# Optimization experiments

Measured on AMD Instinct MI355X. Metric: run time of the kernel, lower is better.

## Reference

```python
import jax, jax.numpy as jnp
import numpy as np

N_NODES = 100000
N_EDGES = 1000000
D_FEAT = 64
N_GRAPHS = 64


def setup_inputs() -> dict:
    key = jax.random.key(0)
    ks = jax.random.split(key, 5)
    x = jax.random.normal(ks[0], (N_NODES, D_FEAT), dtype=jnp.float32)
    edge_index = jax.random.randint(ks[1], (2, N_EDGES), 0, N_NODES, dtype=jnp.int32)
    batch = jnp.sort(jax.random.randint(ks[2], (N_NODES,), 0, N_GRAPHS, dtype=jnp.int32))
    s = 1.0 / np.sqrt(D_FEAT)
    W1 = jax.random.uniform(ks[3], (D_FEAT, D_FEAT), jnp.float32, -s, s)
    W2 = jax.random.uniform(ks[4], (D_FEAT, D_FEAT), jnp.float32, -s, s)
    b1 = jnp.zeros((D_FEAT,), jnp.float32)
    b2 = jnp.zeros((D_FEAT,), jnp.float32)
    return {"x": x, "edge_index": edge_index, "batch": batch,
            "W1": W1, "b1": b1, "W2": W2, "b2": b2}


def gcn_conv(x, edge_index, W, b, num_nodes):
    # PyG GCNConv: h = D^{-1/2} (A + I) D^{-1/2} (x W) + b
    loops = jnp.arange(num_nodes, dtype=edge_index.dtype)
    row = jnp.concatenate([edge_index[0], loops])  # source nodes
    col = jnp.concatenate([edge_index[1], loops])  # target nodes
    h = x @ W  # [N, D]
    deg = jax.ops.segment_sum(jnp.ones_like(col, dtype=h.dtype), col,
                              num_segments=num_nodes)  # >= 1 due to self loops
    dinv = jax.lax.rsqrt(deg)
    norm = dinv[row] * dinv[col]  # [E+N]
    out = jax.ops.segment_sum(h[row] * norm[:, None], col, num_segments=num_nodes)
    return out + b


def reference(x, edge_index, batch, W1, b1, W2, b2):
    n = x.shape[0]
    h = gcn_conv(x, edge_index, W1, b1, n)
    h = gcn_conv(h, edge_index, W2, b2, n)
    # global_mean_pool over graph ids
    sums = jax.ops.segment_sum(h, batch, num_segments=N_GRAPHS)  # [G, D]
    cnts = jax.ops.segment_sum(jnp.ones((n, 1), h.dtype), batch,
                               num_segments=N_GRAPHS)
    return sums / jnp.maximum(cnts, 1.0)
```

## Files before the change

### kernel.cpp

```cpp
#include <hip/hip_runtime.h>
#include <hip/hip_fp16.h>

#define DFEAT 64
#define NG 64
#define TILE 128
#define NBLK 256
#define NBMAX 1024

__global__ __launch_bounds__(256) void k_cnt(const int* __restrict__ col,
                                             int* __restrict__ cnt_m,
                                             float* __restrict__ zeroreg,
                                             const float* __restrict__ x,
                                             __half2* __restrict__ xh,
                                             int e, int nb, int chunk, int n32) {
  __shared__ int hist[NBMAX];
  int tid = threadIdx.x;
  int blk = blockIdx.x;
  if (blk == 0) {
    for (int i = tid; i < 4224; i += 256) zeroreg[i] = 0.f;
  }
  for (int b = tid; b < nb; b += 256) hist[b] = 0;
  __syncthreads();
  int lo = blk * chunk, hi = min(lo + chunk, e);
  for (int i = lo + tid; i < hi; i += 256)
    atomicAdd(&hist[col[i] >> 7], 1);
  __syncthreads();
  for (int b = tid; b < nb; b += 256)
    cnt_m[(size_t)blk * nb + b] = hist[b];
  for (int i = blk * 256 + tid; i < n32; i += NBLK * 256) {
    float2 v = ((const float2*)x)[i];
    xh[i] = __float22half2_rn(v);
  }
}

__global__ __launch_bounds__(256) void k_colscan(int* __restrict__ cnt_m,
                                                 int* __restrict__ gcount, int nb) {
  __shared__ int sh[256];
  int tid = threadIdx.x;
  int b = blockIdx.x;
  int v = cnt_m[(size_t)tid * nb + b];
  sh[tid] = v;
  __syncthreads();
  for (int off = 1; off < 256; off <<= 1) {
    int t = (tid >= off) ? sh[tid - off] : 0;
    __syncthreads();
    sh[tid] += t;
    __syncthreads();
  }
  cnt_m[(size_t)tid * nb + b] = sh[tid] - v;
  if (tid == 255) gcount[b] = sh[255];
}

__global__ __launch_bounds__(1024) void k_bscan(const int* __restrict__ gcount,
                                                int* __restrict__ base, int nb,
                                                const float* __restrict__ W1,
                                                const float* __restrict__ W2,
                                                const float* __restrict__ b1,
                                                float* __restrict__ WW,
                                                float* __restrict__ bw) {
  __shared__ int sh[1024];
  __shared__ float w1[4096], w2[4096];
  int tid = threadIdx.x;
  if (blockIdx.x == 0) {
    int v = (tid < nb) ? gcount[tid] : 0;
    sh[tid] = v;
    __syncthreads();
    for (int off = 1; off < 1024; off <<= 1) {
      int t = (tid >= off) ? sh[tid - off] : 0;
      __syncthreads();
      sh[tid] += t;
      __syncthreads();
    }
    if (tid < nb) base[tid] = sh[tid] - v;
    if (tid == 0) base[nb] = sh[1023];
  } else {
    for (int i = tid; i < 4096; i += 1024) { w1[i] = W1[i]; w2[i] = W2[i]; }
    __syncthreads();
    for (int p = tid; p < 4096; p += 1024) {
      int k = p >> 6, d = p & 63;
      float a = 0.f;
      for (int m = 0; m < 64; ++m) a += w1[k * 64 + m] * w2[m * 64 + d];
      WW[p] = a;
    }
    if (tid < 64) {
      float a = 0.f;
      for (int k = 0; k < 64; ++k) a += b1[k] * w2[k * 64 + tid];
      bw[tid] = a;
    }
  }
}

__global__ __launch_bounds__(256) void k_bin2(const int* __restrict__ row,
                                              const int* __restrict__ col,
                                              const int* __restrict__ base,
                                              const int* __restrict__ cnt_m,
                                              int* __restrict__ pairs,
                                              int e, int nb, int chunk) {
  __shared__ int gl[NBMAX];
  __shared__ int lcur[NBMAX];
  int tid = threadIdx.x;
  int blk = blockIdx.x;
  for (int b = tid; b < nb; b += 256) {
    gl[b] = base[b] + cnt_m[(size_t)blk * nb + b];
    lcur[b] = 0;
  }
  __syncthreads();
  int lo = blk * chunk, hi = min(lo + chunk, e);
  for (int i = lo + tid; i < hi; i += 256) {
    int s = row[i], t = col[i];
    int b = t >> 7;
    int pos = gl[b] + atomicAdd(&lcur[b], 1);
    pairs[pos] = s | ((t & (TILE - 1)) << 20);
  }
}

__global__ __launch_bounds__(256) void k_csr(const int* __restrict__ pairs,
                                             const int* __restrict__ base,
                                             int* __restrict__ starts,
                                             int* __restrict__ srcs,
                                             float* __restrict__ dinv,
                                             int n, int e) {
  __shared__ int cnt[TILE];
  __shared__ int cur[TILE];
  __shared__ int sc[TILE];
  int tid = threadIdx.x;
  int b = blockIdx.x;
  int tile0 = b * TILE;
  if (tid < TILE) cnt[tid] = 0;
  __syncthreads();
  int e0 = base[b], e1 = base[b + 1];
  for (int i = e0 + tid; i < e1; i += 256)
    atomicAdd(&cnt[(unsigned)pairs[i] >> 20], 1);
  __syncthreads();
  int c = (tid < TILE) ? cnt[tid] : 0;
  if (tid < TILE) sc[tid] = c;
  __syncthreads();
  for (int off = 1; off < TILE; off <<= 1) {
    int t = (tid < TILE && tid >= off) ? sc[tid - off] : 0;
    __syncthreads();
    if (tid < TILE) sc[tid] += t;
    __syncthreads();
  }
  if (tid < TILE) {
    int excl = sc[tid] - c;
    cur[tid] = excl;
    int node = tile0 + tid;
    if (node < n) {
      starts[node] = e0 + excl;
      dinv[node] = rsqrtf(1.0f + (float)c);
    }
  }
  if (b == 0 && tid == 0) starts[n] = e;
  __syncthreads();
  for (int i = e0 + tid; i < e1; i += 256) {
    int p = pairs[i];
    int pos = atomicAdd(&cur[(unsigned)p >> 20], 1);
    srcs[e0 + pos] = p & 0xFFFFF;
  }
}

__global__ __launch_bounds__(256) void k_gather1(const int* __restrict__ starts,
                                                 const int* __restrict__ srcs,
                                                 const float* __restrict__ dinv,
                                                 const __half2* __restrict__ xh,
                                                 __half2* __restrict__ z1h,
                                                 float* __restrict__ u, int n) {
  int node = blockIdx.x * 8 + (threadIdx.x >> 5);
  if (node >= n) return;
  int lh = threadIdx.x & 31;
  int s = starts[node];
  int deg = starts[node + 1] - s;
  float dc = dinv[node];
  float2 hs = __half22float2(xh[(size_t)node * 32 + lh]);
  float ax = 0.f, ay = 0.f, wsum = 0.f;
  int j = 0;
  for (; j + 7 < deg; j += 8) {
    int r0 = srcs[s + j + 0], r1 = srcs[s + j + 1];
    int r2 = srcs[s + j + 2], r3 = srcs[s + j + 3];
    int r4 = srcs[s + j + 4], r5 = srcs[s + j + 5];
    int r6 = srcs[s + j + 6], r7 = srcs[s + j + 7];
    float w0 = dinv[r0], w1 = dinv[r1], w2 = dinv[r2], w3 = dinv[r3];
    float w4 = dinv[r4], w5 = dinv[r5], w6 = dinv[r6], w7 = dinv[r7];
    float2 v0 = __half22float2(xh[(size_t)r0 * 32 + lh]);
    float2 v1 = __half22float2(xh[(size_t)r1 * 32 + lh]);
    float2 v2 = __half22float2(xh[(size_t)r2 * 32 + lh]);
    float2 v3 = __half22float2(xh[(size_t)r3 * 32 + lh]);
    float2 v4 = __half22float2(xh[(size_t)r4 * 32 + lh]);
    float2 v5 = __half22float2(xh[(size_t)r5 * 32 + lh]);
    float2 v6 = __half22float2(xh[(size_t)r6 * 32 + lh]);
    float2 v7 = __half22float2(xh[(size_t)r7 * 32 + lh]);
    ax += w0 * v0.x + w1 * v1.x + w2 * v2.x + w3 * v3.x
        + w4 * v4.x + w5 * v5.x + w6 * v6.x + w7 * v7.x;
    ay += w0 * v0.y + w1 * v1.y + w2 * v2.y + w3 * v3.y
        + w4 * v4.y + w5 * v5.y + w6 * v6.y + w7 * v7.y;
    wsum += w0 + w1 + w2 + w3 + w4 + w5 + w6 + w7;
  }
  for (; j < deg; ++j) {
    int r = srcs[s + j];
    float w = dinv[r];
    float2 v = __half22float2(xh[(size_t)r * 32 + lh]);
    ax += w * v.x;
    ay += w * v.y;
    wsum += w;
  }
  float2 res;
  res.x = dc * dc * hs.x + dc * ax;
  res.y = dc * dc * hs.y + dc * ay;
  z1h[(size_t)node * 32 + lh] = __float22half2_rn(res);
  if (lh == 0) u[node] = dc * (dc + wsum);
}

__global__ __launch_bounds__(256) void k_gather2(const int* __restrict__ starts,
                                                 const int* __restrict__ srcs,
                                                 const float* __restrict__ dinv,
                                                 const __half2* __restrict__ z1h,
                                                 float* __restrict__ z2, int n) {
  int node = blockIdx.x * 8 + (threadIdx.x >> 5);
  if (node >= n) return;
  int lh = threadIdx.x & 31;
  int s = starts[node];
  int deg = starts[node + 1] - s;
  float dc = dinv[node];
  float2 hs = __half22float2(z1h[(size_t)node * 32 + lh]);
  float ax = 0.f, ay = 0.f;
  int j = 0;
  for (; j + 7 < deg; j += 8) {
    int r0 = srcs[s + j + 0], r1 = srcs[s + j + 1];
    int r2 = srcs[s + j + 2], r3 = srcs[s + j + 3];
    int r4 = srcs[s + j + 4], r5 = srcs[s + j + 5];
    int r6 = srcs[s + j + 6], r7 = srcs[s + j + 7];
    float w0 = dinv[r0], w1 = dinv[r1], w2 = dinv[r2], w3 = dinv[r3];
    float w4 = dinv[r4], w5 = dinv[r5], w6 = dinv[r6], w7 = dinv[r7];
    float2 v0 = __half22float2(z1h[(size_t)r0 * 32 + lh]);
    float2 v1 = __half22float2(z1h[(size_t)r1 * 32 + lh]);
    float2 v2 = __half22float2(z1h[(size_t)r2 * 32 + lh]);
    float2 v3 = __half22float2(z1h[(size_t)r3 * 32 + lh]);
    float2 v4 = __half22float2(z1h[(size_t)r4 * 32 + lh]);
    float2 v5 = __half22float2(z1h[(size_t)r5 * 32 + lh]);
    float2 v6 = __half22float2(z1h[(size_t)r6 * 32 + lh]);
    float2 v7 = __half22float2(z1h[(size_t)r7 * 32 + lh]);
    ax += w0 * v0.x + w1 * v1.x + w2 * v2.x + w3 * v3.x
        + w4 * v4.x + w5 * v5.x + w6 * v6.x + w7 * v7.x;
    ay += w0 * v0.y + w1 * v1.y + w2 * v2.y + w3 * v3.y
        + w4 * v4.y + w5 * v5.y + w6 * v6.y + w7 * v7.y;
  }
  for (; j < deg; ++j) {
    int r = srcs[s + j];
    float w = dinv[r];
    float2 v = __half22float2(z1h[(size_t)r * 32 + lh]);
    ax += w * v.x;
    ay += w * v.y;
  }
  float2 res;
  res.x = dc * dc * hs.x + dc * ax;
  res.y = dc * dc * hs.y + dc * ay;
  *(float2*)(&z2[(size_t)node * 64 + lh * 2]) = res;
}

__global__ void k_pool2(const float* __restrict__ z2, const float* __restrict__ u,
                        const int* __restrict__ batch, float* __restrict__ S,
                        float* __restrict__ T, float* __restrict__ cntf, int n) {
  int d = threadIdx.x;
  int start = blockIdx.x * 64;
  if (start >= n) return;
  int end = min(start + 64, n);
  int curg = batch[start];
  float acc = 0.f, cnt = 0.f, ua = 0.f;
  for (int i = start; i < end; ++i) {
    int g = batch[i];
    if (g != curg) {
      unsafeAtomicAdd(&S[curg * 64 + d], acc);
      if (d == 0) {
        unsafeAtomicAdd(&cntf[curg], cnt);
        unsafeAtomicAdd(&T[curg], ua);
      }
      acc = 0.f; cnt = 0.f; ua = 0.f;
      curg = g;
    }
    acc += z2[(size_t)i * 64 + d];
    if (d == 0) { cnt += 1.f; ua += u[i]; }
  }
  unsafeAtomicAdd(&S[curg * 64 + d], acc);
  if (d == 0) {
    unsafeAtomicAdd(&cntf[curg], cnt);
    unsafeAtomicAdd(&T[curg], ua);
  }
}

__global__ __launch_bounds__(256) void k_final2(const float* __restrict__ S,
                                                const float* __restrict__ T,
                                                const float* __restrict__ cntf,
                                                const float* __restrict__ WW,
                                                const float* __restrict__ bw,
                                                const float* __restrict__ b2,
                                                float* __restrict__ out) {
  __shared__ float sS[4096], sW[4096];
  int tid = threadIdx.x;
  for (int i = tid; i < 4096; i += 256) { sS[i] = S[i]; sW[i] = WW[i]; }
  __syncthreads();
  for (int p = tid; p < 4096; p += 256) {
    int g = p >> 6, d = p & 63;
    float a = 0.f;
    for (int k = 0; k < 64; ++k) a += sS[g * 64 + k] * sW[k * 64 + d];
    float c = fmaxf(cntf[g], 1.0f);
    out[p] = (a + T[g] * bw[d]) / c + b2[d];
  }
}

extern "C" void kernel_launch(void* const* d_in, const int* in_sizes, int n_in,
                              void* d_out, int out_size, void* d_ws, size_t ws_size,
                              hipStream_t stream) {
  const float* x = (const float*)d_in[0];
  const int* ei = (const int*)d_in[1];
  const int* bat = (const int*)d_in[2];
  const float* W1 = (const float*)d_in[3];
  const float* b1 = (const float*)d_in[4];
  const float* W2 = (const float*)d_in[5];
  const float* b2 = (const float*)d_in[6];
  float* out = (float*)d_out;

  int n = in_sizes[0] / 64;
  int e = in_sizes[1] / 2;
  const int* rowp = ei;
  const int* colp = ei + e;
  int nb = (n + TILE - 1) / TILE;
  int chunk = (e + NBLK - 1) / NBLK;

  char* ws = (char*)d_ws;
  size_t off = 0;
  auto alloc = [&](size_t elems) {
    void* p = ws + off;
    off += ((elems * 4 + 255) & ~(size_t)255);
    return p;
  };
  float* S = (float*)alloc(NG * DFEAT);
  float* cntf = (float*)alloc(NG);
  float* T = (float*)alloc(NG);
  int* gcount = (int*)alloc(nb);
  int* base = (int*)alloc(nb + 1);
  int* cnt_m = (int*)alloc((size_t)NBLK * nb);
  float* dinv = (float*)alloc(n);
  int* starts = (int*)alloc(n + 1);
  int* srcs = (int*)alloc(e);
  float* u = (float*)alloc(n);
  float* WW = (float*)alloc(DFEAT * DFEAT);
  float* bw = (float*)alloc(DFEAT);
  __half2* xh = (__half2*)alloc((size_t)n * 32);
  __half2* z1h = (__half2*)alloc((size_t)n * 32);
  float* z2 = (float*)alloc((size_t)n * 64);
  int* pairs = (int*)z2;

  int nbw = (n + 7) / 8;
  int n32 = n * 32;

  k_cnt<<<NBLK, 256, 0, stream>>>(colp, cnt_m, S, x, xh, e, nb, chunk, n32);
  k_colscan<<<nb, 256, 0, stream>>>(cnt_m, gcount, nb);
  k_bscan<<<2, 1024, 0, stream>>>(gcount, base, nb, W1, W2, b1, WW, bw);
  k_bin2<<<NBLK, 256, 0, stream>>>(rowp, colp, base, cnt_m, pairs, e, nb, chunk);
  k_csr<<<nb, 256, 0, stream>>>(pairs, base, starts, srcs, dinv, n, e);

  k_gather1<<<nbw, 256, 0, stream>>>(starts, srcs, dinv, xh, z1h, u, n);
  k_gather2<<<nbw, 256, 0, stream>>>(starts, srcs, dinv, z1h, z2, n);

  k_pool2<<<(n + 63) / 64, 64, 0, stream>>>(z2, u, bat, S, T, cntf, n);
  k_final2<<<1, 256, 0, stream>>>(S, T, cntf, WW, bw, b2, out);
}
```

Baseline: 237.7 us.

## Fuse second-layer gather with mean-pool reduction via shared-memory staging

Merges the second aggregation kernel and the pooling kernel into one: each 1024-thread block aggregates 32 nodes into shared memory, then 64 threads reduce them per graph and atomically add into the graph sums. This removes the write and re-read of the full fp32 z2 buffer (about 25 MB) and one kernel launch. The pairs scratch now gets its own allocation instead of aliasing z2. The cost is 1024-thread blocks with a barrier, and a serial 32-step pooling loop per block, which may limit occupancy and add atomics.

```diff
diff --git a/kernel.cpp b/kernel.cpp
--- a/kernel.cpp
+++ b/kernel.cpp
@@ -210,78 +210,88 @@
   if (lh == 0) u[node] = dc * (dc + wsum);
 }
 
-__global__ __launch_bounds__(256) void k_gather2(const int* __restrict__ starts,
-                                                 const int* __restrict__ srcs,
-                                                 const float* __restrict__ dinv,
-                                                 const __half2* __restrict__ z1h,
-                                                 float* __restrict__ z2, int n) {
-  int node = blockIdx.x * 8 + (threadIdx.x >> 5);
-  if (node >= n) return;
-  int lh = threadIdx.x & 31;
-  int s = starts[node];
-  int deg = starts[node + 1] - s;
-  float dc = dinv[node];
-  float2 hs = __half22float2(z1h[(size_t)node * 32 + lh]);
-  float ax = 0.f, ay = 0.f;
-  int j = 0;
-  for (; j + 7 < deg; j += 8) {
-    int r0 = srcs[s + j + 0], r1 = srcs[s + j + 1];
-    int r2 = srcs[s + j + 2], r3 = srcs[s + j + 3];
-    int r4 = srcs[s + j + 4], r5 = srcs[s + j + 5];
-    int r6 = srcs[s + j + 6], r7 = srcs[s + j + 7];
-    float w0 = dinv[r0], w1 = dinv[r1], w2 = dinv[r2], w3 = dinv[r3];
-    float w4 = dinv[r4], w5 = dinv[r5], w6 = dinv[r6], w7 = dinv[r7];
-    float2 v0 = __half22float2(z1h[(size_t)r0 * 32 + lh]);
-    float2 v1 = __half22float2(z1h[(size_t)r1 * 32 + lh]);
-    float2 v2 = __half22float2(z1h[(size_t)r2 * 32 + lh]);
-    float2 v3 = __half22float2(z1h[(size_t)r3 * 32 + lh]);
-    float2 v4 = __half22float2(z1h[(size_t)r4 * 32 + lh]);
-    float2 v5 = __half22float2(z1h[(size_t)r5 * 32 + lh]);
-    float2 v6 = __half22float2(z1h[(size_t)r6 * 32 + lh]);
-    float2 v7 = __half22float2(z1h[(size_t)r7 * 32 + lh]);
-    ax += w0 * v0.x + w1 * v1.x + w2 * v2.x + w3 * v3.x
-        + w4 * v4.x + w5 * v5.x + w6 * v6.x + w7 * v7.x;
-    ay += w0 * v0.y + w1 * v1.y + w2 * v2.y + w3 * v3.y
-        + w4 * v4.y + w5 * v5.y + w6 * v6.y + w7 * v7.y;
-  }
-  for (; j < deg; ++j) {
-    int r = srcs[s + j];
-    float w = dinv[r];
-    float2 v = __half22float2(z1h[(size_t)r * 32 + lh]);
-    ax += w * v.x;
-    ay += w * v.y;
-  }
-  float2 res;
-  res.x = dc * dc * hs.x + dc * ax;
-  res.y = dc * dc * hs.y + dc * ay;
-  *(float2*)(&z2[(size_t)node * 64 + lh * 2]) = res;
-}
-
-__global__ void k_pool2(const float* __restrict__ z2, const float* __restrict__ u,
-                        const int* __restrict__ batch, float* __restrict__ S,
-                        float* __restrict__ T, float* __restrict__ cntf, int n) {
-  int d = threadIdx.x;
-  int start = blockIdx.x * 64;
-  if (start >= n) return;
-  int end = min(start + 64, n);
-  int curg = batch[start];
-  float acc = 0.f, cnt = 0.f, ua = 0.f;
-  for (int i = start; i < end; ++i) {
-    int g = batch[i];
-    if (g != curg) {
-      unsafeAtomicAdd(&S[curg * 64 + d], acc);
-      if (d == 0) {
+__global__ __launch_bounds__(1024) void k_gather2p(const int* __restrict__ starts,
+                                                   const int* __restrict__ srcs,
+                                                   const float* __restrict__ dinv,
+                                                   const __half2* __restrict__ z1h,
+                                                   const float* __restrict__ u,
+                                                   const int* __restrict__ batch,
+                                                   float* __restrict__ S,
+                                                   float* __restrict__ T,
+                                                   float* __restrict__ cntf, int n) {
+  __shared__ float zblk[32 * 64];
+  int tid = threadIdx.x;
+  int nl = tid >> 5;
+  int lh = tid & 31;
+  int base0 = blockIdx.x * 32;
+  int node = base0 + nl;
+  if (node < n) {
+    int s = starts[node];
+    int deg = starts[node + 1] - s;
+    float dc = dinv[node];
+    float2 hs = __half22float2(z1h[(size_t)node * 32 + lh]);
+    float ax = 0.f, ay = 0.f;
+    int j = 0;
+    for (; j + 7 < deg; j += 8) {
+      int r0 = srcs[s + j + 0], r1 = srcs[s + j + 1];
+      int r2 = srcs[s + j + 2], r3 = srcs[s + j + 3];
+      int r4 = srcs[s + j + 4], r5 = srcs[s + j + 5];
+      int r6 = srcs[s + j + 6], r7 = srcs[s + j + 7];
+      float w0 = dinv[r0], w1 = dinv[r1], w2 = dinv[r2], w3 = dinv[r3];
+      float w4 = dinv[r4], w5 = dinv[r5], w6 = dinv[r6], w7 = dinv[r7];
+      float2 v0 = __half22float2(z1h[(size_t)r0 * 32 + lh]);
+      float2 v1 = __half22float2(z1h[(size_t)r1 * 32 + lh]);
+      float2 v2 = __half22float2(z1h[(size_t)r2 * 32 + lh]);
+      float2 v3 = __half22float2(z1h[(size_t)r3 * 32 + lh]);
+      float2 v4 = __half22float2(z1h[(size_t)r4 * 32 + lh]);
+      float2 v5 = __half22float2(z1h[(size_t)r5 * 32 + lh]);
+      float2 v6 = __half22float2(z1h[(size_t)r6 * 32 + lh]);
+      float2 v7 = __half22float2(z1h[(size_t)r7 * 32 + lh]);
+      ax += w0 * v0.x + w1 * v1.x + w2 * v2.x + w3 * v3.x
+          + w4 * v4.x + w5 * v5.x + w6 * v6.x + w7 * v7.x;
+      ay += w0 * v0.y + w1 * v1.y + w2 * v2.y + w3 * v3.y
+          + w4 * v4.y + w5 * v5.y + w6 * v6.y + w7 * v7.y;
+    }
+    for (; j < deg; ++j) {
+      int r = srcs[s + j];
+      float w = dinv[r];
+      float2 v = __half22float2(z1h[(size_t)r * 32 + lh]);
+      ax += w * v.x;
+      ay += w * v.y;
+    }
+    zblk[nl * 64 + lh * 2] = dc * dc * hs.x + dc * ax;
+    zblk[nl * 64 + lh * 2 + 1] = dc * dc * hs.y + dc * ay;
+  }
+  __syncthreads();
+  int m = min(32, n - base0);
+  if (m <= 0) return;
+  if (tid < 64) {
+    int curg = batch[base0];
+    float acc = 0.f;
+    for (int i = 0; i < m; ++i) {
+      int g = batch[base0 + i];
+      if (g != curg) {
+        unsafeAtomicAdd(&S[curg * 64 + tid], acc);
+        acc = 0.f;
+        curg = g;
+      }
+      acc += zblk[i * 64 + tid];
+    }
+    unsafeAtomicAdd(&S[curg * 64 + tid], acc);
+  } else if (tid == 64) {
+    int curg = batch[base0];
+    float cnt = 0.f, ua = 0.f;
+    for (int i = 0; i < m; ++i) {
+      int g = batch[base0 + i];
+      if (g != curg) {
         unsafeAtomicAdd(&cntf[curg], cnt);
         unsafeAtomicAdd(&T[curg], ua);
+        cnt = 0.f; ua = 0.f;
+        curg = g;
       }
-      acc = 0.f; cnt = 0.f; ua = 0.f;
-      curg = g;
-    }
-    acc += z2[(size_t)i * 64 + d];
-    if (d == 0) { cnt += 1.f; ua += u[i]; }
-  }
-  unsafeAtomicAdd(&S[curg * 64 + d], acc);
-  if (d == 0) {
+      cnt += 1.f;
+      ua += u[base0 + i];
+    }
     unsafeAtomicAdd(&cntf[curg], cnt);
     unsafeAtomicAdd(&T[curg], ua);
   }
@@ -347,10 +357,10 @@
   float* bw = (float*)alloc(DFEAT);
   __half2* xh = (__half2*)alloc((size_t)n * 32);
   __half2* z1h = (__half2*)alloc((size_t)n * 32);
-  float* z2 = (float*)alloc((size_t)n * 64);
-  int* pairs = (int*)z2;
+  int* pairs = (int*)alloc(e);
 
   int nbw = (n + 7) / 8;
+  int nbp = (n + 31) / 32;
   int n32 = n * 32;
 
   k_cnt<<<NBLK, 256, 0, stream>>>(colp, cnt_m, S, x, xh, e, nb, chunk, n32);
@@ -360,8 +370,7 @@
   k_csr<<<nb, 256, 0, stream>>>(pairs, base, starts, srcs, dinv, n, e);
 
   k_gather1<<<nbw, 256, 0, stream>>>(starts, srcs, dinv, xh, z1h, u, n);
-  k_gather2<<<nbw, 256, 0, stream>>>(starts, srcs, dinv, z1h, z2, n);
-
-  k_pool2<<<(n + 63) / 64, 64, 0, stream>>>(z2, u, bat, S, T, cntf, n);
+  k_gather2p<<<nbp, 1024, 0, stream>>>(starts, srcs, dinv, z1h, u, bat, S, T, cntf, n);
+
   k_final2<<<1, 256, 0, stream>>>(S, T, cntf, WW, bw, b2, out);
 }
```

Result: no change. 235.4 us (-1.0%).
